# Kernel tuning notes

Measured on AMD Instinct MI355X. Metric: run time of the kernel, lower is better.

The kernel has to match this reference:

```python
import jax, jax.numpy as jnp
import numpy as np

N, D, S, H, QP, VP = 512, 256, 32, 4, 8, 8
PAIR_C = S + 3 * VP          # 56
P3 = H * QP * 3              # 96
FD = P3 + 16                 # 112 (rel + dist rbf)


def _layer_norm(x, scale, offset, eps=1e-5):
    mu = x.mean(-1, keepdims=True)
    var = ((x - mu) ** 2).mean(-1, keepdims=True)
    return (x - mu) * jax.lax.rsqrt(var + eps) * scale + offset


def _distance_rbf(d, bins=16, min_d=0.0, max_d=22.0):
    # Gaussian RBF featurization of pairwise distances (salad distance_rbf).
    step = (max_d - min_d) / bins
    centers = min_d + step * jnp.arange(bins, dtype=d.dtype) + step / 2
    return jnp.exp(-(((d[..., None] - centers) / step) ** 2))


def setup_inputs() -> dict:
    key = jax.random.key(0)
    ks = jax.random.split(key, 16)
    f32 = jnp.float32
    nrm = lambda k, shape, s=1.0: (s * jax.random.normal(k, shape)).astype(f32)
    HS = H * S
    return {
        "local": nrm(ks[0], (N, D)),
        "pos": nrm(ks[1], (N, 5, 3)),
        "resi": jnp.arange(N, dtype=jnp.int32),
        "chain": jax.random.randint(ks[2], (N,), 0, 2, dtype=jnp.int32),
        "batch": jnp.zeros((N,), dtype=jnp.int32),
        "mask": jnp.ones((N,), dtype=bool),
        "q_ln_scale": jnp.ones((S,), f32),
        "q_ln_offset": jnp.zeros((S,), f32),
        "k_ln_scale": jnp.ones((S,), f32),
        "k_ln_offset": jnp.zeros((S,), f32),
        "w_q": nrm(ks[3], (D, HS), D ** -0.5),
        "b_q": jnp.zeros((HS,), f32),
        "w_k": nrm(ks[4], (D, HS), D ** -0.5),
        "b_k": jnp.zeros((HS,), f32),
        "w_v": nrm(ks[5], (D, HS), D ** -0.5),
        "b_v": jnp.zeros((HS,), f32),
        "w_qp": nrm(ks[6], (D, H * QP * 3), 0.1 * D ** -0.5),
        "b_qp": jnp.zeros((H * QP * 3,), f32),
        "w_kp": nrm(ks[7], (D, H * QP * 3), 0.1 * D ** -0.5),
        "b_kp": jnp.zeros((H * QP * 3,), f32),
        "w_vp": nrm(ks[8], (D, H * VP * 3), 0.1 * D ** -0.5),
        "b_vp": jnp.zeros((H * VP * 3,), f32),
        "resi_embedding": nrm(ks[9], (66, PAIR_C), 66 ** -0.5),
        "w_pair": nrm(ks[10], (FD, PAIR_C), FD ** -0.5),
        "w_bias": nrm(ks[11], (FD, H), FD ** -0.5),
        "b_bias": jnp.zeros((H,), f32),
        "gamma": jnp.full((H,), np.log(np.e - 1.0), f32),
        "w_out": nrm(ks[12], (H * PAIR_C, D), (H * PAIR_C) ** -0.5),
    }


def reference(local, pos, resi, chain, batch, mask,
              q_ln_scale, q_ln_offset, k_ln_scale, k_ln_offset,
              w_q, b_q, w_k, b_k, w_v, b_v,
              w_qp, b_qp, w_kp, b_kp, w_vp, b_vp,
              resi_embedding, w_pair, w_bias, b_bias, gamma, w_out):
    n = local.shape[0]
    ca = pos[:, 1]  # [n,3]

    q = _layer_norm((local @ w_q + b_q).reshape(n, H, S), q_ln_scale, q_ln_offset)
    k = _layer_norm((local @ w_k + b_k).reshape(n, H, S), k_ln_scale, k_ln_offset)
    v = (local @ w_v + b_v).reshape(n, H, S)
    qp = (local @ w_qp + b_qp).reshape(n, H, QP, 3) + ca[:, None, None]
    kp = (local @ w_kp + b_kp).reshape(n, H, QP, 3) + ca[:, None, None]
    vp = (local @ w_vp + b_vp).reshape(n, H, VP, 3) + ca[:, None, None]
    value = jnp.concatenate((v, vp.reshape(n, H, 3 * VP)), axis=-1)  # [n,H,56]

    same_batch = batch[:, None] == batch[None, :]
    pair_mask = (mask[:, None] & mask[None, :]) & same_batch  # [n,n]

    inner = jnp.einsum('ihc,jhc->ijh', q * jnp.sqrt(1.0 / S), k)  # [n,n,H]
    diff = qp[:, None] - kp[None, :]                 # [n,n,H,QP,3]
    point_att = -(diff ** 2).sum(axis=(-1, -2))      # [n,n,H]
    rel = diff.reshape(n, n, P3)                     # [n,n,96]

    dca = 10.0 * ca
    dist = jnp.sqrt(((dca[:, None] - dca[None, :]) ** 2).sum(-1) + 1e-6)
    dist = _distance_rbf(dist)                       # [n,n,16]

    resi_dist = jnp.clip(resi[:, None] - resi[None, :], -32, 32)
    other_chain = chain[:, None] != chain[None, :]
    rdist = jnp.where(other_chain, 65, resi_dist + 32)
    emb = resi_embedding[rdist]                      # [n,n,56]

    feat = jnp.concatenate((rel, dist), axis=-1)     # [n,n,112]
    pair = emb + feat @ w_pair                       # [n,n,56]
    bias = feat @ w_bias + b_bias                    # [n,n,H]
    pair = pair[:, :, None, :] + value[None]         # [n,n,H,56]

    w_C = jnp.sqrt(2.0 / (9 * QP))
    point_scale = jax.nn.softplus(gamma).reshape(1, 1, H) * w_C / 2

    attn = (inner + point_scale * point_att + bias) * jnp.sqrt(1.0 / 3.0)
    attn = jnp.where(pair_mask[..., None], attn, -1e9)
    attn = jax.nn.softmax(attn, axis=1)
    attn = jnp.where(pair_mask[..., None], attn, 0.0)

    result = jnp.einsum('ijh,ijhc->ihc', attn, pair).reshape(n, -1)  # [n,224]
    return result @ w_out                             # [n,D]
```

## Files before the change

### kernel.cpp

```cpp
#include <hip/hip_runtime.h>
#include <hip/hip_bf16.h>
#include <cstddef>

#define N_NODES 512
#define DIM     256
#define H_HEADS 4
#define PAIR_CN 56
#define P3_N    96
#define FD_N    112
#define HPC     224

typedef _Float16 h2v __attribute__((ext_vector_type(2)));

__device__ __forceinline__ bool mask_true(const void* m, int idx) {
    if (((const unsigned char*)m)[idx] != 0) return true;
    return ((const int*)m)[idx] != 0;
}
__device__ __forceinline__ unsigned packh2(float a, float b) {
    _Float16 ha = (_Float16)a, hb = (_Float16)b;
    unsigned short ua, ub;
    __builtin_memcpy(&ua, &ha, 2); __builtin_memcpy(&ub, &hb, 2);
    return (unsigned)ua | ((unsigned)ub << 16);
}
__device__ __forceinline__ float h2lof(unsigned u) {
    unsigned short t = (unsigned short)(u & 0xffff);
    _Float16 h; __builtin_memcpy(&h, &t, 2); return (float)h;
}
__device__ __forceinline__ float h2hif(unsigned u) {
    unsigned short t = (unsigned short)(u >> 16);
    _Float16 h; __builtin_memcpy(&h, &t, 2); return (float)h;
}
__device__ __forceinline__ float dot2u(unsigned a, unsigned b, float c) {
#if __has_builtin(__builtin_amdgcn_fdot2)
    h2v ha, hb;
    __builtin_memcpy(&ha, &a, 4);
    __builtin_memcpy(&hb, &b, 4);
    return __builtin_amdgcn_fdot2(ha, hb, c, false);
#else
    return c + h2lof(a)*h2lof(b) + h2hif(a)*h2hif(b);
#endif
}

__global__ __launch_bounds__(512) void proj_kernel(
    const float* __restrict__ local, const float* __restrict__ pos,
    const float* __restrict__ qls, const float* __restrict__ qlo,
    const float* __restrict__ kls, const float* __restrict__ klo,
    const float* __restrict__ w_q, const float* __restrict__ b_q,
    const float* __restrict__ w_k, const float* __restrict__ b_k,
    const float* __restrict__ w_v, const float* __restrict__ b_v,
    const float* __restrict__ w_qp, const float* __restrict__ b_qp,
    const float* __restrict__ w_kp, const float* __restrict__ b_kp,
    const float* __restrict__ w_vp, const float* __restrict__ b_vp,
    const float* __restrict__ w_bias, const float* __restrict__ b_bias,
    const float* __restrict__ gamma,
    const float* __restrict__ remb, const float* __restrict__ w_pair,
    const float* __restrict__ w_out,
    unsigned* __restrict__ qnP, unsigned* __restrict__ knT4,
    unsigned* __restrict__ qpP, unsigned* __restrict__ kpT4,
    unsigned* __restrict__ valT2, unsigned* __restrict__ kpT2,
    unsigned* __restrict__ woPk, unsigned* __restrict__ wp2,
    unsigned* __restrict__ remb2,
    float* __restrict__ jinfo, float* __restrict__ iinfo)
{
    const int i0 = blockIdx.x * 2;
    const int tid = threadIdx.x;

    __shared__ float xL[2][DIM];
    __shared__ float qraw[2][128];
    __shared__ float kraw[2][128];
    __shared__ float stat[2][16];
    __shared__ float qpL[2][P3_N];
    __shared__ float kpbL[2][P3_N];
    __shared__ float wbS[384];

    if (blockIdx.x < 16) {
        for (int t = blockIdx.x*512 + tid; t < 33656; t += 8192) {
            if (t < 28672) {
                const int t2 = t >> 8, colx = t & 255;
                woPk[t] = packh2(w_out[(size_t)(2*t2)*DIM + colx],
                                 w_out[(size_t)(2*t2 + 1)*DIM + colx]);
            } else if (t < 31808) {
                const int v = t - 28672, f2 = v / 56, cx = v % 56;
                wp2[v] = packh2(w_pair[(2*f2)*PAIR_CN + cx],
                                w_pair[(2*f2 + 1)*PAIR_CN + cx]);
            } else {
                const int v = t - 31808, r2 = v / 56, cx = v % 56;
                remb2[v] = packh2(remb[(2*r2)*PAIR_CN + cx],
                                  remb[(2*r2 + 1)*PAIR_CN + cx]);
            }
        }
    }

    {
        const int r = tid >> 8, d = tid & 255;
        xL[r][d] = local[(size_t)(i0 + r) * DIM + d];
    }
    if (tid < 384) wbS[tid] = w_bias[tid];
    __syncthreads();

    char* valT2B = (char*)valT2;
    char* kpT2B  = (char*)kpT2;
    const size_t jp = (size_t)(i0 >> 1);

    if (tid < 336) {
        const int colg = tid >> 1, dh = tid & 1;
        const int col = colg * 4;
        const float* w; int width, c, seg;
        if      (col < 128) { w = w_q;  c = col;       width = 128; seg = 0; }
        else if (col < 256) { w = w_k;  c = col - 128; width = 128; seg = 1; }
        else if (col < 384) { w = w_v;  c = col - 256; width = 128; seg = 2; }
        else if (col < 480) { w = w_qp; c = col - 384; width = 96;  seg = 3; }
        else if (col < 576) { w = w_kp; c = col - 480; width = 96;  seg = 4; }
        else                { w = w_vp; c = col - 576; width = 96;  seg = 5; }

        float acc[2][4] = {{0.f,0.f,0.f,0.f},{0.f,0.f,0.f,0.f}};
#pragma unroll 4
        for (int dd = 0; dd < 128; ++dd) {
            const int d = dh*128 + dd;
            float4 wv = *(const float4*)(w + (size_t)d * width + c);
#pragma unroll
            for (int r = 0; r < 2; ++r) {
                float x = xL[r][d];
                acc[r][0] += x * wv.x; acc[r][1] += x * wv.y;
                acc[r][2] += x * wv.z; acc[r][3] += x * wv.w;
            }
        }
#pragma unroll
        for (int r = 0; r < 2; ++r)
#pragma unroll
            for (int e = 0; e < 4; ++e)
                acc[r][e] += __shfl_xor(acc[r][e], 1);

        if (dh == 0) {
            const float cax0 = pos[i0*15+3],     cay0 = pos[i0*15+4],     caz0 = pos[i0*15+5];
            const float cax1 = pos[(i0+1)*15+3], cay1 = pos[(i0+1)*15+4], caz1 = pos[(i0+1)*15+5];
            float fr0[4], fr1[4];
            const bool isKp = (seg == 4), isQp = (seg == 3);
#pragma unroll
            for (int e = 0; e < 4; ++e) {
                const int cc = c + e;
                const float v0 = acc[0][e], v1 = acc[1][e];
                if (seg == 0) {
                    qraw[0][cc] = v0 + b_q[cc];
                    qraw[1][cc] = v1 + b_q[cc];
                } else if (seg == 1) {
                    kraw[0][cc] = v0 + b_k[cc];
                    kraw[1][cc] = v1 + b_k[cc];
                } else if (seg == 2) {
                    const int h = cc >> 5, sc = cc & 31;
                    const int row = h*PAIR_CN + sc;
                    *(unsigned*)(valT2B + jp*896 + row*4) =
                        packh2(v0 + b_v[cc], v1 + b_v[cc]);
                } else if (seg == 3) {
                    const int x = cc % 3;
                    const float cav0 = (x==0)?cax0:((x==1)?cay0:caz0);
                    const float cav1 = (x==0)?cax1:((x==1)?cay1:caz1);
                    const float r0 = v0 + b_qp[cc] + cav0;
                    const float r1 = v1 + b_qp[cc] + cav1;
                    fr0[e] = r0; fr1[e] = r1;
                    qpL[0][cc] = r0; qpL[1][cc] = r1;
                } else if (seg == 4) {
                    const int x = cc % 3;
                    const float cav0 = (x==0)?cax0:((x==1)?cay0:caz0);
                    const float cav1 = (x==0)?cax1:((x==1)?cay1:caz1);
                    const float r0 = v0 + b_kp[cc] + cav0;
                    const float r1 = v1 + b_kp[cc] + cav1;
                    fr0[e] = r0; fr1[e] = r1;
                    *(unsigned*)(kpT2B + jp*384 + cc*4) = packh2(r0, r1);
                    kpbL[0][cc] = (float)(_Float16)r0;
                    kpbL[1][cc] = (float)(_Float16)r1;
                } else {
                    const int h = cc / 24, rr = cc % 24, x = cc % 3;
                    const float cav0 = (x==0)?cax0:((x==1)?cay0:caz0);
                    const float cav1 = (x==0)?cax1:((x==1)?cay1:caz1);
                    const int row = h*PAIR_CN + 32 + rr;
                    *(unsigned*)(valT2B + jp*896 + row*4) =
                        packh2(v0 + b_vp[cc] + cav0, v1 + b_vp[cc] + cav1);
                }
            }
            if (isQp) {
                const int f2 = c >> 1;
                qpP[(size_t)i0*48 + f2]         = packh2(fr0[0], fr0[1]);
                qpP[(size_t)i0*48 + f2 + 1]     = packh2(fr0[2], fr0[3]);
                qpP[(size_t)(i0+1)*48 + f2]     = packh2(fr1[0], fr1[1]);
                qpP[(size_t)(i0+1)*48 + f2 + 1] = packh2(fr1[2], fr1[3]);
            }
            if (isKp) {
                const int f2 = c >> 1;
                const int fq = f2 >> 2;
                kpT4[((size_t)fq*N_NODES + i0    )*4 + (f2 & 3)]       = packh2(fr0[0], fr0[1]);
                kpT4[((size_t)fq*N_NODES + i0    )*4 + ((f2 + 1) & 3)] = packh2(fr0[2], fr0[3]);
                kpT4[((size_t)fq*N_NODES + i0 + 1)*4 + (f2 & 3)]       = packh2(fr1[0], fr1[1]);
                kpT4[((size_t)fq*N_NODES + i0 + 1)*4 + ((f2 + 1) & 3)] = packh2(fr1[2], fr1[3]);
            }
        }
    }
    __syncthreads();

    if (tid < 16) {
        const int r = tid >> 3, t = tid & 7;
        const float* src = (t < 4) ? qraw[r] : kraw[r];
        const int h = t & 3, base = (t < 4) ? 0 : 8;
        float mu = 0.f;
        for (int c = 0; c < 32; ++c) mu += src[h*32 + c];
        mu *= (1.f/32.f);
        float var = 0.f;
        for (int c = 0; c < 32; ++c) { float d = src[h*32 + c] - mu; var += d*d; }
        var *= (1.f/32.f);
        stat[r][base + h*2 + 0] = mu;
        stat[r][base + h*2 + 1] = var;
    }
    __syncthreads();

    {
        const int r = tid >> 8, u = tid & 255;
        const int i = i0 + r;
        if (u < 128) {
            const int h = u >> 5, sidx = u & 31;
            const float mu = stat[r][h*2], var = stat[r][h*2+1];
            float v = (qraw[r][u] - mu) * rsqrtf(var + 1e-5f) * qls[sidx] + qlo[sidx];
            v *= 0.17677669529663687f;
            const float vo = __shfl_xor(v, 1);
            if (!(u & 1)) qnP[(size_t)i*64 + (u >> 1)] = packh2(v, vo);
        } else {
            const int u2 = u - 128, h = u2 >> 5, sidx = u2 & 31;
            const float mu = stat[r][8 + h*2], var = stat[r][9 + h*2];
            float v = (kraw[r][u2] - mu) * rsqrtf(var + 1e-5f) * kls[sidx] + klo[sidx];
            const float vo = __shfl_xor(v, 1);
            if (!(u2 & 1))
                knT4[(((size_t)(u2 >> 3))*N_NODES + i)*4 + ((u2 >> 1) & 3)] = packh2(v, vo);
        }
    }

    if (tid < 64) {
        const int r = tid >> 5, h = (tid >> 3) & 3, ks = tid & 7;
        float uacc = 0.f, tacc = 0.f;
#pragma unroll
        for (int f = ks; f < P3_N; f += 8) {
            float wb = wbS[f*4 + h];
            uacc += qpL[r][f] * wb;
            tacc += kpbL[r][f] * wb;
        }
        float nq = 0.f, nk = 0.f;
#pragma unroll
        for (int f = h*24 + ks*3; f < h*24 + ks*3 + 3; ++f) {
            nq += qpL[r][f]*qpL[r][f];
            nk += kpbL[r][f]*kpbL[r][f];
        }
        uacc += __shfl_xor(uacc,1); uacc += __shfl_xor(uacc,2); uacc += __shfl_xor(uacc,4);
        tacc += __shfl_xor(tacc,1); tacc += __shfl_xor(tacc,2); tacc += __shfl_xor(tacc,4);
        nq   += __shfl_xor(nq,1);   nq   += __shfl_xor(nq,2);   nq   += __shfl_xor(nq,4);
        nk   += __shfl_xor(nk,1);   nk   += __shfl_xor(nk,2);   nk   += __shfl_xor(nk,4);
        if (ks == 0) {
            const int n = i0 + r;
            const float ps = log1pf(expf(gamma[h])) * (1.0f/12.0f);
            iinfo[n*4 + h] = -ps*nq + uacc + b_bias[h];
            jinfo[n*8 + h] = -ps*nk - tacc;
            if (h == 0) {
                jinfo[n*8 + 4] = 10.f * pos[n*15 + 3];
                jinfo[n*8 + 5] = 10.f * pos[n*15 + 4];
                jinfo[n*8 + 6] = 10.f * pos[n*15 + 5];
                jinfo[n*8 + 7] = 0.f;
            }
        }
    }
}

__global__ __launch_bounds__(512, 4) void attn_kernel(
    const unsigned* __restrict__ qnP, const unsigned* __restrict__ knT4,
    const unsigned* __restrict__ qpP, const unsigned* __restrict__ kpT4,
    const unsigned* __restrict__ valT2, const unsigned* __restrict__ kpT2,
    const unsigned* __restrict__ woPk, const unsigned* __restrict__ wp2,
    const unsigned* __restrict__ remb2,
    const float* __restrict__ jinfo, const float* __restrict__ iinfo,
    const int* __restrict__ resi, const int* __restrict__ chain,
    const int* __restrict__ batch, const void* __restrict__ maskp,
    const float* __restrict__ w_bias, const float* __restrict__ gamma,
    float* __restrict__ out)
{
    const int i    = blockIdx.x;
    const int tid  = threadIdx.x;
    const int lane = tid & 63;
    const int wv   = tid >> 6;

    __shared__ unsigned qpkL[64];
    __shared__ unsigned qspkL[48];
    __shared__ unsigned wbPk[H_HEADS][8];
    __shared__ unsigned rbfP[N_NODES][9];
    __shared__ unsigned attnH[H_HEADS][260];
    __shared__ float    mxW[8][H_HEADS], smW[8][H_HEADS];
    __shared__ float    asL[H_HEADS];
    __shared__ float    qpiL[P3_N];
    __shared__ float    partR[4][56][4];
    __shared__ float    partG[8][P3_N][4];
    __shared__ float    GLfR[H_HEADS][16];
    __shared__ unsigned GLf2[H_HEADS][56];
    __shared__ unsigned abktP[H_HEADS][33];
    __shared__ float    resL[HPC];
    __shared__ unsigned resH[FD_N];
    __shared__ float    abkt2[2][H_HEADS][66];
    __shared__ unsigned char rdL[N_NODES], pmL[N_NODES];

    if (tid < 64) {
        qpkL[tid] = qnP[(size_t)i*64 + tid];
    } else if (tid < 112) {
        const int f2 = tid - 64, h = f2 / 12;
        const float ps2 = 2.f * log1pf(expf(gamma[h])) * (1.0f/12.0f);
        const unsigned u = qpP[(size_t)i*48 + f2];
        qspkL[f2] = packh2(ps2*h2lof(u), ps2*h2hif(u));
    } else if (tid < 160) {
        const int f2 = tid - 112;
        const unsigned u = qpP[(size_t)i*48 + f2];
        qpiL[2*f2]   = h2lof(u);
        qpiL[2*f2+1] = h2hif(u);
    } else if (tid < 192) {
        const int v = tid - 160, h = v >> 3, e = v & 7;
        wbPk[h][e] = packh2(w_bias[(P3_N + 2*e)*H_HEADS + h],
                            w_bias[(P3_N + 2*e + 1)*H_HEADS + h]);
    }
    for (int t = tid; t < 2*H_HEADS*66; t += 512) ((float*)abkt2)[t] = 0.f;

    const int  r_i = resi[i], ch_i = chain[i], ba_i = batch[i];
    const bool m_i = mask_true(maskp, i);
    const float dix = jinfo[(size_t)i*8+4], diy = jinfo[(size_t)i*8+5], diz = jinfo[(size_t)i*8+6];

    const float inv3  = 0.57735026918962576f;
    const float rstep = 0.72727272727272727f;

    const int j = tid;
    const float4 vq4 = *(const float4*)(jinfo + (size_t)j*8);
    const float4 dj4 = *(const float4*)(jinfo + (size_t)j*8 + 4);
    const float4 ci4 = *(const float4*)(iinfo + (size_t)i*4);
    const float vqa[4] = {vq4.x, vq4.y, vq4.z, vq4.w};
    const float cia[4] = {ci4.x, ci4.y, ci4.z, ci4.w};
    const float dd0 = dix - dj4.x, dd1 = diy - dj4.y, dd2 = diz - dj4.z;
    const float dist = sqrtf(dd0*dd0 + dd1*dd1 + dd2*dd2 + 1e-6f);
    unsigned rr[8];
#pragma unroll
    for (int p = 0; p < 8; ++p) {
        const float u0 = (dist - (1.375f*(float)(2*p)   + 0.6875f)) * rstep;
        const float u1 = (dist - (1.375f*(float)(2*p+1) + 0.6875f)) * rstep;
        rr[p] = packh2(__expf(-u0*u0), __expf(-u1*u1));
        rbfP[j][p] = rr[p];
    }
    const int  rj = resi[j], cj = chain[j], bj = batch[j];
    const bool pm = m_i && mask_true(maskp, j) && (ba_i == bj);
    rdL[j] = (unsigned char)((ch_i != cj) ? 65 : (min(max(r_i - rj, -32), 32) + 32));
    pmL[j] = pm ? 1 : 0;
    __syncthreads();

    float lv[4];
    {
        const uint4* kcol = (const uint4*)knT4 + j;
        const uint4* pcol = (const uint4*)kpT4 + j;
        const uint4* qk4  = (const uint4*)qpkL;
        const uint4* qs4  = (const uint4*)qspkL;
#pragma unroll
        for (int h = 0; h < 4; ++h) {
            float acc = 0.f;
#pragma unroll
            for (int g = 0; g < 4; ++g) {
                const uint4 kk = kcol[(size_t)(h*4 + g)*N_NODES];
                const uint4 qq = qk4[h*4 + g];
                acc = dot2u(kk.x, qq.x, acc);
                acc = dot2u(kk.y, qq.y, acc);
                acc = dot2u(kk.z, qq.z, acc);
                acc = dot2u(kk.w, qq.w, acc);
            }
#pragma unroll
            for (int g = 0; g < 3; ++g) {
                const uint4 kk = pcol[(size_t)(h*3 + g)*N_NODES];
                const uint4 qq = qs4[h*3 + g];
                acc = dot2u(kk.x, qq.x, acc);
                acc = dot2u(kk.y, qq.y, acc);
                acc = dot2u(kk.z, qq.z, acc);
                acc = dot2u(kk.w, qq.w, acc);
            }
            const uint4 w0 = *(const uint4*)&wbPk[h][0];
            const uint4 w1 = *(const uint4*)&wbPk[h][4];
            acc = dot2u(rr[0], w0.x, acc);
            acc = dot2u(rr[1], w0.y, acc);
            acc = dot2u(rr[2], w0.z, acc);
            acc = dot2u(rr[3], w0.w, acc);
            acc = dot2u(rr[4], w1.x, acc);
            acc = dot2u(rr[5], w1.y, acc);
            acc = dot2u(rr[6], w1.z, acc);
            acc = dot2u(rr[7], w1.w, acc);
            lv[h] = pm ? (acc + cia[h] + vqa[h]) * inv3 : -1e9f;
        }
    }

    {
        float mx[4] = {lv[0], lv[1], lv[2], lv[3]};
#pragma unroll
        for (int off = 1; off < 64; off <<= 1) {
#pragma unroll
            for (int h = 0; h < 4; ++h) mx[h] = fmaxf(mx[h], __shfl_xor(mx[h], off));
        }
        if (lane == 0) *(float4*)&mxW[wv][0] = make_float4(mx[0], mx[1], mx[2], mx[3]);
        __syncthreads();
        float mxg[4] = {-1e30f, -1e30f, -1e30f, -1e30f};
#pragma unroll
        for (int w = 0; w < 8; ++w) {
            const float4 m = *(const float4*)&mxW[w][0];
            mxg[0] = fmaxf(mxg[0], m.x); mxg[1] = fmaxf(mxg[1], m.y);
            mxg[2] = fmaxf(mxg[2], m.z); mxg[3] = fmaxf(mxg[3], m.w);
        }
        float e[4], sm[4];
#pragma unroll
        for (int h = 0; h < 4; ++h) {
            e[h] = pm ? __expf(lv[h] - mxg[h]) : 0.f;
            sm[h] = e[h];
        }
#pragma unroll
        for (int off = 1; off < 64; off <<= 1) {
#pragma unroll
            for (int h = 0; h < 4; ++h) sm[h] += __shfl_xor(sm[h], off);
        }
        if (lane == 0) *(float4*)&smW[wv][0] = make_float4(sm[0], sm[1], sm[2], sm[3]);
        __syncthreads();
        float smt[4] = {0.f, 0.f, 0.f, 0.f};
#pragma unroll
        for (int w = 0; w < 8; ++w) {
            const float4 m = *(const float4*)&smW[w][0];
            smt[0] += m.x; smt[1] += m.y; smt[2] += m.z; smt[3] += m.w;
        }
        const int half = j >> 8;
        float p[4];
#pragma unroll
        for (int h = 0; h < 4; ++h) {
            const float rden = 1.f / fmaxf(smt[h], 1e-37f);
            p[h] = e[h] * rden;
            atomicAdd(&abkt2[half][h][rdL[j]], p[h]);
        }
        if (tid == 0) {
#pragma unroll
            for (int h = 0; h < 4; ++h)
                asL[h] = smt[h] / fmaxf(smt[h], 1e-37f);
        }
#pragma unroll
        for (int h = 0; h < 4; ++h) {
            const float po = __shfl_xor(p[h], 1);
            if (!(j & 1)) attnH[h][j >> 1] = packh2(p[h], po);
        }
    }
    __syncthreads();

    if (tid < 224) {
        const int g = tid % 56, q = tid / 56;
        const int h = g / 14;
        const char* colp = (const char*)valT2 + g*16;
        float a0 = 0.f, a1 = 0.f, a2 = 0.f, a3 = 0.f;
#pragma unroll 8
        for (int jpq = q*64; jpq < q*64 + 64; ++jpq) {
            const uint4 u = *(const uint4*)(colp + (size_t)jpq*896);
            const unsigned pw = attnH[h][jpq];
            a0 = dot2u(u.x, pw, a0);
            a1 = dot2u(u.y, pw, a1);
            a2 = dot2u(u.z, pw, a2);
            a3 = dot2u(u.w, pw, a3);
        }
        partR[q][g][0] = a0; partR[q][g][1] = a1;
        partR[q][g][2] = a2; partR[q][g][3] = a3;
    } else if (tid < 416) {
        const int v = tid - 224, g = v % 24, e = v / 24;
        const char* colp = (const char*)kpT2 + g*16;
        float a[16];
#pragma unroll
        for (int k = 0; k < 16; ++k) a[k] = 0.f;
#pragma unroll 4
        for (int jpq = e*32; jpq < e*32 + 32; ++jpq) {
            const uint4 u = *(const uint4*)(colp + (size_t)jpq*384);
#pragma unroll
            for (int h = 0; h < 4; ++h) {
                const unsigned pw = attnH[h][jpq];
                a[0*4 + h] = dot2u(u.x, pw, a[0*4 + h]);
                a[1*4 + h] = dot2u(u.y, pw, a[1*4 + h]);
                a[2*4 + h] = dot2u(u.z, pw, a[2*4 + h]);
                a[3*4 + h] = dot2u(u.w, pw, a[3*4 + h]);
            }
        }
#pragma unroll
        for (int fi = 0; fi < 4; ++fi)
#pragma unroll
            for (int h = 0; h < 4; ++h)
                partG[e][g*4 + fi][h] = a[fi*4 + h];
    } else if (tid < 480) {
        const int idx = tid - 416, b = idx >> 2, q = idx & 3;
        const int w = b >> 1;
        const bool hi = (b & 1);
        float a[4] = {0.f, 0.f, 0.f, 0.f};
#pragma unroll 4
        for (int jpp = q*64; jpp < q*64 + 64; ++jpp) {
            const unsigned r0 = rbfP[2*jpp][w];
            const unsigned r1 = rbfP[2*jpp + 1][w];
            const unsigned ee = hi ? ((r0 >> 16) | (r1 & 0xffff0000u))
                                   : ((r0 & 0xffffu) | (r1 << 16));
            a[0] = dot2u(ee, attnH[0][jpp], a[0]);
            a[1] = dot2u(ee, attnH[1][jpp], a[1]);
            a[2] = dot2u(ee, attnH[2][jpp], a[2]);
            a[3] = dot2u(ee, attnH[3][jpp], a[3]);
        }
#pragma unroll
        for (int h = 0; h < 4; ++h) {
            a[h] += __shfl_xor(a[h], 1);
            a[h] += __shfl_xor(a[h], 2);
            if (q == 0) GLfR[h][b] = a[h];
        }
    }
    __syncthreads();

    for (int t = tid; t < 224; t += 512) {
        const int g = t >> 2, e = t & 3;
        resL[t] = partR[0][g][e] + partR[1][g][e] + partR[2][g][e] + partR[3][g][e];
    }
    for (int t = tid; t < 224; t += 512) {
        const int h = t / 56, f2 = t % 56;
        if (f2 < 48) {
            float s0 = 0.f, s1 = 0.f;
#pragma unroll
            for (int e = 0; e < 8; ++e) {
                s0 += partG[e][2*f2][h];
                s1 += partG[e][2*f2 + 1][h];
            }
            GLf2[h][f2] = packh2(qpiL[2*f2]*asL[h] - s0, qpiL[2*f2 + 1]*asL[h] - s1);
        } else {
            GLf2[h][f2] = packh2(GLfR[h][(f2 - 48)*2], GLfR[h][(f2 - 48)*2 + 1]);
        }
    }
    for (int t = tid; t < 132; t += 512) {
        const int h = t / 33, r2 = t % 33;
        abktP[h][r2] = packh2(abkt2[0][h][2*r2]   + abkt2[1][h][2*r2],
                              abkt2[0][h][2*r2+1] + abkt2[1][h][2*r2+1]);
    }
    __syncthreads();

    if (tid < HPC) {
        const int h = tid / PAIR_CN, c = tid - h*PAIR_CN;
        float r = resL[tid];
#pragma unroll 8
        for (int r2 = 0; r2 < 33; ++r2)
            r = dot2u(remb2[r2*56 + c], abktP[h][r2], r);
#pragma unroll 8
        for (int f2 = 0; f2 < 56; ++f2)
            r = dot2u(wp2[f2*56 + c], GLf2[h][f2], r);
        resL[tid] = r;
    }
    __syncthreads();

    if (tid < FD_N) resH[tid] = packh2(resL[2*tid], resL[2*tid + 1]);
    __syncthreads();

    {
        const int col = tid >> 1, ph = tid & 1;
        float o = 0.f;
#pragma unroll 7
        for (int t2 = ph*56; t2 < ph*56 + 56; ++t2)
            o = dot2u(woPk[t2*256 + col], resH[t2], o);
        o += __shfl_xor(o, 1);
        if (ph == 0) out[(size_t)i*DIM + col] = o;
    }
}

extern "C" void kernel_launch(void* const* d_in, const int* in_sizes, int n_in,
                              void* d_out, int out_size, void* d_ws, size_t ws_size,
                              hipStream_t stream) {
    (void)in_sizes; (void)n_in; (void)out_size; (void)ws_size;
    const float* local = (const float*)d_in[0];
    const float* pos   = (const float*)d_in[1];
    const int*   resi  = (const int*)d_in[2];
    const int*   chain = (const int*)d_in[3];
    const int*   batch = (const int*)d_in[4];
    const void*  maskp = d_in[5];
    const float* qls   = (const float*)d_in[6];
    const float* qlo   = (const float*)d_in[7];
    const float* kls   = (const float*)d_in[8];
    const float* klo   = (const float*)d_in[9];
    const float* w_q   = (const float*)d_in[10];
    const float* b_q   = (const float*)d_in[11];
    const float* w_k   = (const float*)d_in[12];
    const float* b_k   = (const float*)d_in[13];
    const float* w_v   = (const float*)d_in[14];
    const float* b_v   = (const float*)d_in[15];
    const float* w_qp  = (const float*)d_in[16];
    const float* b_qp  = (const float*)d_in[17];
    const float* w_kp  = (const float*)d_in[18];
    const float* b_kp  = (const float*)d_in[19];
    const float* w_vp  = (const float*)d_in[20];
    const float* b_vp  = (const float*)d_in[21];
    const float* remb  = (const float*)d_in[22];
    const float* w_pair= (const float*)d_in[23];
    const float* w_bias= (const float*)d_in[24];
    const float* b_bias= (const float*)d_in[25];
    const float* gamma = (const float*)d_in[26];
    const float* w_out = (const float*)d_in[27];

    char* ws = (char*)d_ws;
    unsigned* qnP   = (unsigned*)(ws);
    unsigned* qpP   = (unsigned*)(ws + 131072);
    unsigned* knT4  = (unsigned*)(ws + 229376);
    unsigned* kpT4  = (unsigned*)(ws + 360448);
    unsigned* valT2 = (unsigned*)(ws + 458752);
    unsigned* kpT2  = (unsigned*)(ws + 688128);
    float*    jinf  = (float*)(ws + 786432);
    float*    iinf  = (float*)(ws + 802816);
    unsigned* woPk  = (unsigned*)(ws + 811008);
    unsigned* wp2   = (unsigned*)(ws + 925696);
    unsigned* remb2 = (unsigned*)(ws + 938240);

    proj_kernel<<<N_NODES / 2, 512, 0, stream>>>(
        local, pos, qls, qlo, kls, klo,
        w_q, b_q, w_k, b_k, w_v, b_v,
        w_qp, b_qp, w_kp, b_kp, w_vp, b_vp,
        w_bias, b_bias, gamma,
        remb, w_pair, w_out,
        qnP, knT4, qpP, kpT4, valT2, kpT2,
        woPk, wp2, remb2, jinf, iinf);

    attn_kernel<<<N_NODES, 512, 0, stream>>>(
        qnP, knT4, qpP, kpT4, valT2, kpT2,
        woPk, wp2, remb2, jinf, iinf,
        resi, chain, batch, maskp,
        w_bias, gamma,
        (float*)d_out);
}
```

Measured before the change: 57.41 us.

## Use MFMA 16x16x32 f16 for attention-weighted value and key-point reductions

Replaces the scalar fdot2 reductions of attention weights against value and key-point columns with MFMA f16 matrix instructions run by seven waves. The proj kernel now writes the value and key-point data into a fragment-ready layout (BF) so each lane loads one uint4 per k-tile. Only 4 of the 16 MFMA rows hold data, since there are 4 heads, so most of the matrix unit's work is wasted. In exchange the partial-sum buffers and their cross-thread reduction are removed. The new layout indexing and the remapped thread roles raise correctness risk.

```diff
diff --git a/kernel.cpp b/kernel.cpp
--- a/kernel.cpp
+++ b/kernel.cpp
@@ -10,7 +10,9 @@
 #define FD_N    112
 #define HPC     224
 
-typedef _Float16 h2v __attribute__((ext_vector_type(2)));
+typedef _Float16 h2v  __attribute__((ext_vector_type(2)));
+typedef _Float16 f16x8 __attribute__((ext_vector_type(8)));
+typedef float    f32x4 __attribute__((ext_vector_type(4)));
 
 __device__ __forceinline__ bool mask_true(const void* m, int idx) {
     if (((const unsigned char*)m)[idx] != 0) return true;
@@ -39,6 +41,12 @@
 #else
     return c + h2lof(a)*h2lof(b) + h2hif(a)*h2hif(b);
 #endif
+}
+__device__ __forceinline__ f32x4 mfma16(uint4 a, uint4 b, f32x4 c) {
+    f16x8 af, bf;
+    __builtin_memcpy(&af, &a, 16);
+    __builtin_memcpy(&bf, &b, 16);
+    return __builtin_amdgcn_mfma_f32_16x16x32_f16(af, bf, c, 0, 0, 0);
 }
 
 __global__ __launch_bounds__(512) void proj_kernel(
@@ -57,7 +65,7 @@
     const float* __restrict__ w_out,
     unsigned* __restrict__ qnP, unsigned* __restrict__ knT4,
     unsigned* __restrict__ qpP, unsigned* __restrict__ kpT4,
-    unsigned* __restrict__ valT2, unsigned* __restrict__ kpT2,
+    unsigned* __restrict__ BF,
     unsigned* __restrict__ woPk, unsigned* __restrict__ wp2,
     unsigned* __restrict__ remb2,
     float* __restrict__ jinfo, float* __restrict__ iinfo)
@@ -98,9 +106,7 @@
     if (tid < 384) wbS[tid] = w_bias[tid];
     __syncthreads();
 
-    char* valT2B = (char*)valT2;
-    char* kpT2B  = (char*)kpT2;
-    const size_t jp = (size_t)(i0 >> 1);
+    const int cstBF = ((i0 >> 5) << 8) + (((i0 >> 3) & 3) << 6) + ((i0 >> 1) & 3);
 
     if (tid < 336) {
         const int colg = tid >> 1, dh = tid & 1;
@@ -148,8 +154,8 @@
                     kraw[1][cc] = v1 + b_k[cc];
                 } else if (seg == 2) {
                     const int h = cc >> 5, sc = cc & 31;
-                    const int row = h*PAIR_CN + sc;
-                    *(unsigned*)(valT2B + jp*896 + row*4) =
+                    const int colF = h*PAIR_CN + sc;
+                    BF[(colF >> 4)*4096 + (colF & 15)*4 + cstBF] =
                         packh2(v0 + b_v[cc], v1 + b_v[cc]);
                 } else if (seg == 3) {
                     const int x = cc % 3;
@@ -166,15 +172,16 @@
                     const float r0 = v0 + b_kp[cc] + cav0;
                     const float r1 = v1 + b_kp[cc] + cav1;
                     fr0[e] = r0; fr1[e] = r1;
-                    *(unsigned*)(kpT2B + jp*384 + cc*4) = packh2(r0, r1);
+                    const int colF = 224 + cc;
+                    BF[(colF >> 4)*4096 + (colF & 15)*4 + cstBF] = packh2(r0, r1);
                     kpbL[0][cc] = (float)(_Float16)r0;
                     kpbL[1][cc] = (float)(_Float16)r1;
                 } else {
                     const int h = cc / 24, rr = cc % 24, x = cc % 3;
                     const float cav0 = (x==0)?cax0:((x==1)?cay0:caz0);
                     const float cav1 = (x==0)?cax1:((x==1)?cay1:caz1);
-                    const int row = h*PAIR_CN + 32 + rr;
-                    *(unsigned*)(valT2B + jp*896 + row*4) =
+                    const int colF = h*PAIR_CN + 32 + rr;
+                    BF[(colF >> 4)*4096 + (colF & 15)*4 + cstBF] =
                         packh2(v0 + b_vp[cc] + cav0, v1 + b_vp[cc] + cav1);
                 }
             }
@@ -269,7 +276,7 @@
 __global__ __launch_bounds__(512, 4) void attn_kernel(
     const unsigned* __restrict__ qnP, const unsigned* __restrict__ knT4,
     const unsigned* __restrict__ qpP, const unsigned* __restrict__ kpT4,
-    const unsigned* __restrict__ valT2, const unsigned* __restrict__ kpT2,
+    const unsigned* __restrict__ BF,
     const unsigned* __restrict__ woPk, const unsigned* __restrict__ wp2,
     const unsigned* __restrict__ remb2,
     const float* __restrict__ jinfo, const float* __restrict__ iinfo,
@@ -286,13 +293,12 @@
     __shared__ unsigned qpkL[64];
     __shared__ unsigned qspkL[48];
     __shared__ unsigned wbPk[H_HEADS][8];
-    __shared__ unsigned rbfP[N_NODES][9];
-    __shared__ unsigned attnH[H_HEADS][260];
+    __shared__ __align__(16) unsigned rbfP[N_NODES][9];
+    __shared__ __align__(16) unsigned attnH[H_HEADS][260];
     __shared__ float    mxW[8][H_HEADS], smW[8][H_HEADS];
     __shared__ float    asL[H_HEADS];
     __shared__ float    qpiL[P3_N];
-    __shared__ float    partR[4][56][4];
-    __shared__ float    partG[8][P3_N][4];
+    __shared__ float    GLfF[H_HEADS][P3_N];
     __shared__ float    GLfR[H_HEADS][16];
     __shared__ unsigned GLf2[H_HEADS][56];
     __shared__ unsigned abktP[H_HEADS][33];
@@ -446,47 +452,46 @@
     }
     __syncthreads();
 
-    if (tid < 224) {
-        const int g = tid % 56, q = tid / 56;
-        const int h = g / 14;
-        const char* colp = (const char*)valT2 + g*16;
-        float a0 = 0.f, a1 = 0.f, a2 = 0.f, a3 = 0.f;
-#pragma unroll 8
-        for (int jpq = q*64; jpq < q*64 + 64; ++jpq) {
-            const uint4 u = *(const uint4*)(colp + (size_t)jpq*896);
-            const unsigned pw = attnH[h][jpq];
-            a0 = dot2u(u.x, pw, a0);
-            a1 = dot2u(u.y, pw, a1);
-            a2 = dot2u(u.z, pw, a2);
-            a3 = dot2u(u.w, pw, a3);
-        }
-        partR[q][g][0] = a0; partR[q][g][1] = a1;
-        partR[q][g][2] = a2; partR[q][g][3] = a3;
-    } else if (tid < 416) {
-        const int v = tid - 224, g = v % 24, e = v / 24;
-        const char* colp = (const char*)kpT2 + g*16;
-        float a[16];
-#pragma unroll
-        for (int k = 0; k < 16; ++k) a[k] = 0.f;
+    if (wv < 7) {
+        const int row = lane & 15;
+        const int ntA = wv, ntB = wv + 7, ntC = wv + 14;
+        const bool hasC = (ntC < 20);
+        f32x4 accA = {0.f,0.f,0.f,0.f};
+        f32x4 accB = {0.f,0.f,0.f,0.f};
+        f32x4 accC = {0.f,0.f,0.f,0.f};
+        const uint4* bfp = (const uint4*)BF;
 #pragma unroll 4
-        for (int jpq = e*32; jpq < e*32 + 32; ++jpq) {
-            const uint4 u = *(const uint4*)(colp + (size_t)jpq*384);
-#pragma unroll
-            for (int h = 0; h < 4; ++h) {
-                const unsigned pw = attnH[h][jpq];
-                a[0*4 + h] = dot2u(u.x, pw, a[0*4 + h]);
-                a[1*4 + h] = dot2u(u.y, pw, a[1*4 + h]);
-                a[2*4 + h] = dot2u(u.z, pw, a[2*4 + h]);
-                a[3*4 + h] = dot2u(u.w, pw, a[3*4 + h]);
-            }
-        }
-#pragma unroll
-        for (int fi = 0; fi < 4; ++fi)
-#pragma unroll
-            for (int h = 0; h < 4; ++h)
-                partG[e][g*4 + fi][h] = a[fi*4 + h];
-    } else if (tid < 480) {
-        const int idx = tid - 416, b = idx >> 2, q = idx & 3;
+        for (int kt = 0; kt < 16; ++kt) {
+            uint4 au = make_uint4(0u, 0u, 0u, 0u);
+            if (row < 4) au = *(const uint4*)&attnH[row][kt*16 + (lane >> 4)*4];
+            const uint4 bA = bfp[(ntA*16 + kt)*64 + lane];
+            const uint4 bB = bfp[(ntB*16 + kt)*64 + lane];
+            accA = mfma16(au, bA, accA);
+            accB = mfma16(au, bB, accB);
+            if (hasC) {
+                const uint4 bC = bfp[(ntC*16 + kt)*64 + lane];
+                accC = mfma16(au, bC, accC);
+            }
+        }
+        if (lane < 16) {
+            {
+                const int s = ntA*16 + lane, h = s / PAIR_CN;
+                resL[s] = (h==0) ? accA[0] : ((h==1) ? accA[1] : ((h==2) ? accA[2] : accA[3]));
+            }
+            {
+                const int s = ntB*16 + lane, h = s / PAIR_CN;
+                resL[s] = (h==0) ? accB[0] : ((h==1) ? accB[1] : ((h==2) ? accB[2] : accB[3]));
+            }
+            if (hasC) {
+                const int f = (ntC - 14)*16 + lane;
+                GLfF[0][f] = accC[0];
+                GLfF[1][f] = accC[1];
+                GLfF[2][f] = accC[2];
+                GLfF[3][f] = accC[3];
+            }
+        }
+    } else {
+        const int idx = tid - 448, b = idx >> 2, q = idx & 3;
         const int w = b >> 1;
         const bool hi = (b & 1);
         float a[4] = {0.f, 0.f, 0.f, 0.f};
@@ -511,19 +516,10 @@
     __syncthreads();
 
     for (int t = tid; t < 224; t += 512) {
-        const int g = t >> 2, e = t & 3;
-        resL[t] = partR[0][g][e] + partR[1][g][e] + partR[2][g][e] + partR[3][g][e];
-    }
-    for (int t = tid; t < 224; t += 512) {
         const int h = t / 56, f2 = t % 56;
         if (f2 < 48) {
-            float s0 = 0.f, s1 = 0.f;
-#pragma unroll
-            for (int e = 0; e < 8; ++e) {
-                s0 += partG[e][2*f2][h];
-                s1 += partG[e][2*f2 + 1][h];
-            }
-            GLf2[h][f2] = packh2(qpiL[2*f2]*asL[h] - s0, qpiL[2*f2 + 1]*asL[h] - s1);
+            GLf2[h][f2] = packh2(qpiL[2*f2]*asL[h]     - GLfF[h][2*f2],
+                                 qpiL[2*f2 + 1]*asL[h] - GLfF[h][2*f2 + 1]);
         } else {
             GLf2[h][f2] = packh2(GLfR[h][(f2 - 48)*2], GLfR[h][(f2 - 48)*2 + 1]);
         }
@@ -600,8 +596,7 @@
     unsigned* qpP   = (unsigned*)(ws + 131072);
     unsigned* knT4  = (unsigned*)(ws + 229376);
     unsigned* kpT4  = (unsigned*)(ws + 360448);
-    unsigned* valT2 = (unsigned*)(ws + 458752);
-    unsigned* kpT2  = (unsigned*)(ws + 688128);
+    unsigned* BF    = (unsigned*)(ws + 458752);
     float*    jinf  = (float*)(ws + 786432);
     float*    iinf  = (float*)(ws + 802816);
     unsigned* woPk  = (unsigned*)(ws + 811008);
@@ -614,11 +609,11 @@
         w_qp, b_qp, w_kp, b_kp, w_vp, b_vp,
         w_bias, b_bias, gamma,
         remb, w_pair, w_out,
-        qnP, knT4, qpP, kpT4, valT2, kpT2,
+        qnP, knT4, qpP, kpT4, BF,
         woPk, wp2, remb2, jinf, iinf);
 
     attn_kernel<<<N_NODES, 512, 0, stream>>>(
-        qnP, knT4, qpP, kpT4, valT2, kpT2,
+        qnP, knT4, qpP, kpT4, BF,
         woPk, wp2, remb2, jinf, iinf,
         resi, chain, batch, maskp,
         w_bias, gamma,
```

Result: no change. 56.81 us (-1.0%).
